# Performance work log

Hardware: AMD Instinct MI355X
Metric: run time of the kernel (lower is better)

The kernel has to match this reference:

```python
import jax, jax.numpy as jnp
import numpy as np

N = 100000       # nodes
E = 1600000      # edges (before self-loops)
IN = 32          # input_dim
HID = 64         # hidden_dim
HEADS = 4
HO = HID // HEADS  # per-head out of gat1
OUT = 32         # output_dim
HID2 = HID // 2
BN_EPS = 1e-5
NEG_SLOPE = 0.2  # PyG GATConv default leaky relu slope


def setup_inputs() -> dict:
    key = jax.random.key(0)
    ks = jax.random.split(key, 28)
    f32 = jnp.float32
    rn = lambda k, s, sc=0.1: jax.random.normal(k, s, f32) * sc
    inp = {}
    inp["x"] = jax.random.normal(ks[0], (N, IN), f32)
    inp["edge_index"] = jax.random.randint(ks[1], (2, E), 0, N, jnp.int32)
    # GATConv 1: in=IN, heads=HEADS, out/head=HO, concat
    inp["W1"] = rn(ks[2], (IN, HEADS * HO))
    inp["att_src1"] = rn(ks[3], (HEADS, HO))
    inp["att_dst1"] = rn(ks[4], (HEADS, HO))
    inp["b1"] = rn(ks[5], (HEADS * HO,))
    # GATConv 2: in=HID, heads=1, out=OUT, no concat (mean)
    inp["W2"] = rn(ks[6], (HID, OUT))
    inp["att_src2"] = rn(ks[7], (1, OUT))
    inp["att_dst2"] = rn(ks[8], (1, OUT))
    inp["b2"] = rn(ks[9], (OUT,))
    # BatchNorms (inference mode: running stats)
    inp["bn1_g"] = jnp.ones((HID,), f32)
    inp["bn1_b"] = jnp.zeros((HID,), f32)
    inp["bn1_m"] = rn(ks[10], (HID,), 0.1)
    inp["bn1_v"] = jax.random.uniform(ks[11], (HID,), f32, 0.5, 1.5)
    inp["bn2_g"] = jnp.ones((OUT,), f32)
    inp["bn2_b"] = jnp.zeros((OUT,), f32)
    inp["bn2_m"] = rn(ks[12], (OUT,), 0.1)
    inp["bn2_v"] = jax.random.uniform(ks[13], (OUT,), f32, 0.5, 1.5)
    # classifier: OUT -> HID2 -> 3
    inp["cls_w1"] = rn(ks[14], (OUT, HID2))
    inp["cls_b1"] = rn(ks[15], (HID2,))
    inp["cls_w2"] = rn(ks[16], (HID2, 3))
    inp["cls_b2"] = rn(ks[17], (3,))
    inp["reg_w1"] = rn(ks[18], (OUT, HID2))
    inp["reg_b1"] = rn(ks[19], (HID2,))
    inp["reg_w2"] = rn(ks[20], (HID2, 1))
    inp["reg_b2"] = rn(ks[21], (1,))
    return inp


def _segment_softmax(e, seg, n):
    # e: [E, H]; softmax over edges sharing the same destination segment
    m = jax.ops.segment_max(e, seg, num_segments=n)
    ex = jnp.exp(e - m[seg])
    s = jax.ops.segment_sum(ex, seg, num_segments=n)
    return ex / (s[seg] + 1e-16)


def _gat(x, src, dst, W, a_src, a_dst, b, heads, ho, concat):
    n = x.shape[0]
    h = (x @ W).reshape(n, heads, ho)                    # [N,H,F]
    e = (h * a_src).sum(-1)[src] + (h * a_dst).sum(-1)[dst]  # [E,H]
    e = jax.nn.leaky_relu(e, NEG_SLOPE)
    alpha = _segment_softmax(e, dst, n)                  # [E,H]
    out = jax.ops.segment_sum(h[src] * alpha[:, :, None], dst, num_segments=n)
    out = out.reshape(n, heads * ho) if concat else out.mean(axis=1)
    return out + b


def _bn(x, g, b, m, v):
    return (x - m) * jax.lax.rsqrt(v + BN_EPS) * g + b


def reference(x, edge_index, W1, att_src1, att_dst1, b1, W2, att_src2, att_dst2, b2,
              bn1_g, bn1_b, bn1_m, bn1_v, bn2_g, bn2_b, bn2_m, bn2_v,
              cls_w1, cls_b1, cls_w2, cls_b2, reg_w1, reg_b1, reg_w2, reg_b2):
    n = x.shape[0]
    # PyG GATConv default add_self_loops=True
    loops = jnp.arange(n, dtype=edge_index.dtype)
    src = jnp.concatenate([edge_index[0], loops])
    dst = jnp.concatenate([edge_index[1], loops])

    h = _gat(x, src, dst, W1, att_src1, att_dst1, b1, HEADS, HO, True)   # [N, HID]
    h = jax.nn.relu(_bn(h, bn1_g, bn1_b, bn1_m, bn1_v))
    emb = _gat(h, src, dst, W2, att_src2, att_dst2, b2, 1, OUT, False)   # [N, OUT]
    emb = jax.nn.relu(_bn(emb, bn2_g, bn2_b, bn2_m, bn2_v))

    roles = jax.nn.relu(emb @ cls_w1 + cls_b1) @ cls_w2 + cls_b2          # [N, 3]
    energy = jax.nn.relu(emb @ reg_w1 + reg_b1) @ reg_w2 + reg_b2         # [N, 1]
    return emb, roles, energy
```

## Files before the change

kernel.cpp:

```cpp
#include <hip/hip_runtime.h>
#include <hip/hip_bf16.h>

#define NN 100000
#define EE 1600000
#define ETOT (EE + NN)
#define IND 32
#define HIDD 64
#define NHEADS 4
#define OUTD 32
#define HID2D 32

#define BSH 8
#define NBUCK 391
#define CAP 5120
#define EPB 2048
#define NBBIN ((ETOT + EPB - 1) / EPB)
#define NBLIN1 (NN / 8)

typedef unsigned int uint;

__device__ __forceinline__ uint pack2(float a, float b) {
  uint lo = (uint)__bfloat16_as_ushort(__float2bfloat16(a));
  uint hi = (uint)__bfloat16_as_ushort(__float2bfloat16(b));
  return (hi << 16) | lo;
}
__device__ __forceinline__ float lo2f(uint w) { return __uint_as_float(w << 16); }
__device__ __forceinline__ float hi2f(uint w) { return __uint_as_float(w & 0xFFFF0000u); }

__global__ __launch_bounds__(256) void k_pre(
    const int* __restrict__ ei, int* __restrict__ bcur, int* __restrict__ bins,
    const float* __restrict__ x, const float* __restrict__ W1,
    const float* __restrict__ atsrc, const float* __restrict__ atdst,
    uint* __restrict__ h1u, float* __restrict__ as1, float* __restrict__ ad1) {
  __shared__ int cnt[NBUCK];
  __shared__ float Ws[IND * HIDD];
  __shared__ float xs[8 * IND];
  __shared__ float atS[HIDD], atD[HIDD];
  int t = threadIdx.x;
  if (blockIdx.x < NBBIN) {
    for (int i = t; i < NBUCK; i += 256) cnt[i] = 0;
    __syncthreads();
    int base = blockIdx.x * EPB;
    int recs[8], bks[8];
#pragma unroll
    for (int k = 0; k < 8; k++) {
      int i = base + k * 256 + t;
      recs[k] = -1; bks[k] = 0;
      if (i < ETOT) {
        int s, d;
        if (i < EE) { s = ei[i]; d = ei[EE + i]; } else { s = i - EE; d = s; }
        recs[k] = (s << BSH) | (d & ((1 << BSH) - 1));
        bks[k] = d >> BSH;
        atomicAdd(&cnt[bks[k]], 1);
      }
    }
    __syncthreads();
    for (int i = t; i < NBUCK; i += 256) cnt[i] = atomicAdd(&bcur[i], cnt[i]);
    __syncthreads();
#pragma unroll
    for (int k = 0; k < 8; k++) {
      if (recs[k] >= 0) {
        int pos = atomicAdd(&cnt[bks[k]], 1);
        bins[bks[k] * CAP + pos] = recs[k];
      }
    }
  } else {
    int bid = blockIdx.x - NBBIN;
    for (int i = t; i < IND * HIDD; i += 256) Ws[i] = W1[i];
    if (t < HIDD) { atS[t] = atsrc[t]; atD[t] = atdst[t]; }
    xs[t] = x[bid * 256 + t];
    __syncthreads();
    int nl = t >> 5, tl = t & 31;
    int node = bid * 8 + nl;
    int j0 = 2 * tl, j1 = j0 + 1;
    float a0 = 0.f, a1 = 0.f;
#pragma unroll
    for (int k = 0; k < IND; k++) {
      float xv = xs[nl * IND + k];
      a0 += xv * Ws[k * HIDD + j0];
      a1 += xv * Ws[k * HIDD + j1];
    }
    h1u[node * 32 + tl] = pack2(a0, a1);
    float ps = a0 * atS[j0] + a1 * atS[j1];
    float pd = a0 * atD[j0] + a1 * atD[j1];
#pragma unroll
    for (int off = 4; off >= 1; off >>= 1) {
      ps += __shfl_down(ps, off, 8);
      pd += __shfl_down(pd, off, 8);
    }
    if ((tl & 7) == 0) {
      as1[node * NHEADS + (tl >> 3)] = ps;
      ad1[node * NHEADS + (tl >> 3)] = pd;
    }
  }
}

__global__ __launch_bounds__(256) void k_lin2(
    const float* __restrict__ hbn, const float* __restrict__ W2,
    const float* __restrict__ atsrc, const float* __restrict__ atdst,
    uint* __restrict__ h2u, float* __restrict__ as2, float* __restrict__ ad2) {
  __shared__ float Ws[HIDD * OUTD];
  __shared__ float xs[16 * HIDD];
  __shared__ float atS[OUTD], atD[OUTD];
  int t = threadIdx.x;
  for (int i = t; i < HIDD * OUTD; i += 256) Ws[i] = W2[i];
  if (t < OUTD) { atS[t] = atsrc[t]; atD[t] = atdst[t]; }
  for (int i = t; i < 16 * HIDD; i += 256) xs[i] = hbn[blockIdx.x * 16 * HIDD + i];
  __syncthreads();
  int nl = t >> 4, tl = t & 15;
  int node = blockIdx.x * 16 + nl;
  int j0 = 2 * tl, j1 = j0 + 1;
  float a0 = 0.f, a1 = 0.f;
#pragma unroll
  for (int k = 0; k < HIDD; k++) {
    float xv = xs[nl * HIDD + k];
    a0 += xv * Ws[k * OUTD + j0];
    a1 += xv * Ws[k * OUTD + j1];
  }
  h2u[node * 16 + tl] = pack2(a0, a1);
  float ps = a0 * atS[j0] + a1 * atS[j1];
  float pd = a0 * atD[j0] + a1 * atD[j1];
#pragma unroll
  for (int off = 8; off >= 1; off >>= 1) {
    ps += __shfl_down(ps, off, 16);
    pd += __shfl_down(pd, off, 16);
  }
  if (tl == 0) { as2[node] = ps; ad2[node] = pd; }
}

__global__ __launch_bounds__(256) void k_csr(const int* __restrict__ bcur,
                                             const int* __restrict__ bins,
                                             int* __restrict__ rowp,
                                             int* __restrict__ srcs) {
  __shared__ int lrec[CAP];
  __shared__ int sA[512], sB[512];
  __shared__ int ldeg[256];
  int b = blockIdx.x, t = threadIdx.x;
  if (b == 0) {
    if (t < 64) srcs[ETOT + t] = 0;
    if (t == 0) rowp[NN] = ETOT;
  }
  sA[t] = (t < NBUCK) ? bcur[t] : 0;
  sA[t + 256] = (t + 256 < NBUCK) ? bcur[t + 256] : 0;
  __syncthreads();
  int* in = sA; int* out = sB;
  for (int off = 1; off < 512; off <<= 1) {
    for (int i = t; i < 512; i += 256)
      out[i] = in[i] + ((i >= off) ? in[i - off] : 0);
    __syncthreads();
    int* tmp = in; in = out; out = tmp;
  }
  int gb = (b == 0) ? 0 : in[b - 1];
  __syncthreads();
  int count = bcur[b]; if (count > CAP) count = CAP;
  ldeg[t] = 0;
  __syncthreads();
  for (int i = t; i < count; i += 256) {
    int r = bins[b * CAP + i];
    lrec[i] = r;
    atomicAdd(&ldeg[r & 255], 1);
  }
  __syncthreads();
  int dv = ldeg[t];
  sA[t] = dv;
  __syncthreads();
  in = sA; out = sB;
  for (int off = 1; off < 256; off <<= 1) {
    out[t] = in[t] + ((t >= off) ? in[t - off] : 0);
    __syncthreads();
    int* tmp = in; in = out; out = tmp;
  }
  int nb = b << BSH;
  int ex = in[t] - dv;
  if (nb + t < NN) rowp[nb + t] = gb + ex;
  ldeg[t] = ex;
  __syncthreads();
  for (int i = t; i < count; i += 256) {
    int r = lrec[i];
    int pos = atomicAdd(&ldeg[r & 255], 1);
    srcs[gb + pos] = (r >> BSH) << 3;
  }
}

__global__ __launch_bounds__(256, 4) void k_agg1(
    const int* __restrict__ rowp, const int* __restrict__ srcs,
    const uint* __restrict__ h1u, const float* __restrict__ as1,
    const float* __restrict__ ad1, const float* __restrict__ b1,
    const float* __restrict__ g, const float* __restrict__ bb,
    const float* __restrict__ m, const float* __restrict__ v,
    float* __restrict__ hbn) {
  int t = threadIdx.x;
  int wid = t >> 6, lane = t & 63;
  int nA = blockIdx.x * 8 + wid * 2;
  int nB = nA + 1;
  int slot = lane >> 3;
  int fl = lane & 7;
  int hd = fl >> 1;
  int stA = rowp[nA], eA = rowp[nA + 1], eB = rowp[nB + 1];
  int stB = eA;
  float advA = ad1[nA * NHEADS + hd];
  float advB = ad1[nB * NHEADS + hd];
  const uint4* h14 = (const uint4*)h1u;
  float accA[8] = {0,0,0,0,0,0,0,0}, accB[8] = {0,0,0,0,0,0,0,0};
  float lA = 0.f, lB = 0.f;
  int pA = stA + slot, pB = stB + slot;
  int sA0 = srcs[pA];
  int sB0 = srcs[pB];
  uint4 wA = h14[sA0 + fl];
  uint4 wB = h14[sB0 + fl];
  float asA = as1[(sA0 >> 1) + hd];
  float asB = as1[(sB0 >> 1) + hd];
  int p1A = pA + 8, p1B = pB + 8;
  int sA1 = srcs[p1A];
  int sB1 = srcs[p1B];
  while (pA < eA || pB < eB) {
    uint4 wnA = h14[sA1 + fl];
    uint4 wnB = h14[sB1 + fl];
    float anA = as1[(sA1 >> 1) + hd];
    float anB = as1[(sB1 >> 1) + hd];
    int p2A = p1A + 8, p2B = p1B + 8;
    int sA2 = srcs[p2A < ETOT ? p2A : ETOT];
    int sB2 = srcs[p2B < ETOT ? p2B : ETOT];
    if (pA < eA) {
      float e = asA + advA;
      e = fmaxf(e, 0.2f * e);
      float ex = __expf(e);
      lA += ex;
      accA[0] += ex * lo2f(wA.x); accA[1] += ex * hi2f(wA.x);
      accA[2] += ex * lo2f(wA.y); accA[3] += ex * hi2f(wA.y);
      accA[4] += ex * lo2f(wA.z); accA[5] += ex * hi2f(wA.z);
      accA[6] += ex * lo2f(wA.w); accA[7] += ex * hi2f(wA.w);
    }
    if (pB < eB) {
      float e = asB + advB;
      e = fmaxf(e, 0.2f * e);
      float ex = __expf(e);
      lB += ex;
      accB[0] += ex * lo2f(wB.x); accB[1] += ex * hi2f(wB.x);
      accB[2] += ex * lo2f(wB.y); accB[3] += ex * hi2f(wB.y);
      accB[4] += ex * lo2f(wB.z); accB[5] += ex * hi2f(wB.z);
      accB[6] += ex * lo2f(wB.w); accB[7] += ex * hi2f(wB.w);
    }
    wA = wnA; wB = wnB; asA = anA; asB = anB;
    sA1 = sA2; sB1 = sB2;
    pA = p1A; pB = p1B; p1A = p2A; p1B = p2B;
  }
#pragma unroll
  for (int off = 8; off <= 32; off <<= 1) {
#pragma unroll
    for (int i = 0; i < 8; i++) {
      accA[i] += __shfl_xor(accA[i], off, 64);
      accB[i] += __shfl_xor(accB[i], off, 64);
    }
    lA += __shfl_xor(lA, off, 64);
    lB += __shfl_xor(lB, off, 64);
  }
  if (slot < 2) {
    int node = slot == 0 ? nA : nB;
    float lsum = slot == 0 ? lA : lB;
    float li = 1.f / (lsum + 1e-16f);
    int fb = fl * 8;
    float o[8];
#pragma unroll
    for (int i = 0; i < 8; i++) {
      int j = fb + i;
      float av = slot == 0 ? accA[i] : accB[i];
      float ov = av * li + b1[j];
      ov = (ov - m[j]) * rsqrtf(v[j] + 1e-5f) * g[j] + bb[j];
      o[i] = fmaxf(ov, 0.f);
    }
    float4* dst = (float4*)(hbn + node * HIDD + fb);
    dst[0] = make_float4(o[0], o[1], o[2], o[3]);
    dst[1] = make_float4(o[4], o[5], o[6], o[7]);
  }
}

__global__ __launch_bounds__(256, 4) void k_agg2(
    const int* __restrict__ rowp, const int* __restrict__ srcs,
    const uint* __restrict__ h2u, const float* __restrict__ as2,
    const float* __restrict__ ad2, const float* __restrict__ b2v,
    const float* __restrict__ g, const float* __restrict__ bb,
    const float* __restrict__ m, const float* __restrict__ v,
    float* __restrict__ out_emb) {
  int t = threadIdx.x;
  int wid = t >> 6, lane = t & 63;
  int nA = blockIdx.x * 8 + wid * 2;
  int nB = nA + 1;
  int slot = lane >> 3;
  int fl = lane & 7;
  int stA = rowp[nA], eA = rowp[nA + 1], eB = rowp[nB + 1];
  int stB = eA;
  float advA = ad2[nA], advB = ad2[nB];
  const uint2* h22 = (const uint2*)h2u;
  float accA[4] = {0,0,0,0}, accB[4] = {0,0,0,0};
  float lA = 0.f, lB = 0.f;
  int pA = stA + slot, pB = stB + slot;
  int sA0 = srcs[pA];
  int sB0 = srcs[pB];
  uint2 wA = h22[sA0 + fl];
  uint2 wB = h22[sB0 + fl];
  float asA = as2[sA0 >> 3], asB = as2[sB0 >> 3];
  int p1A = pA + 8, p1B = pB + 8;
  int sA1 = srcs[p1A];
  int sB1 = srcs[p1B];
  while (pA < eA || pB < eB) {
    uint2 wnA = h22[sA1 + fl];
    uint2 wnB = h22[sB1 + fl];
    float anA = as2[sA1 >> 3], anB = as2[sB1 >> 3];
    int p2A = p1A + 8, p2B = p1B + 8;
    int sA2 = srcs[p2A < ETOT ? p2A : ETOT];
    int sB2 = srcs[p2B < ETOT ? p2B : ETOT];
    if (pA < eA) {
      float e = asA + advA;
      e = fmaxf(e, 0.2f * e);
      float ex = __expf(e);
      lA += ex;
      accA[0] += ex * lo2f(wA.x); accA[1] += ex * hi2f(wA.x);
      accA[2] += ex * lo2f(wA.y); accA[3] += ex * hi2f(wA.y);
    }
    if (pB < eB) {
      float e = asB + advB;
      e = fmaxf(e, 0.2f * e);
      float ex = __expf(e);
      lB += ex;
      accB[0] += ex * lo2f(wB.x); accB[1] += ex * hi2f(wB.x);
      accB[2] += ex * lo2f(wB.y); accB[3] += ex * hi2f(wB.y);
    }
    wA = wnA; wB = wnB; asA = anA; asB = anB;
    sA1 = sA2; sB1 = sB2;
    pA = p1A; pB = p1B; p1A = p2A; p1B = p2B;
  }
#pragma unroll
  for (int off = 8; off <= 32; off <<= 1) {
#pragma unroll
    for (int i = 0; i < 4; i++) {
      accA[i] += __shfl_xor(accA[i], off, 64);
      accB[i] += __shfl_xor(accB[i], off, 64);
    }
    lA += __shfl_xor(lA, off, 64);
    lB += __shfl_xor(lB, off, 64);
  }
  if (slot < 2) {
    int node = slot == 0 ? nA : nB;
    float lsum = slot == 0 ? lA : lB;
    float li = 1.f / (lsum + 1e-16f);
    int fb = fl * 4;
    float o[4];
#pragma unroll
    for (int i = 0; i < 4; i++) {
      int j = fb + i;
      float av = slot == 0 ? accA[i] : accB[i];
      float ov = av * li + b2v[j];
      ov = (ov - m[j]) * rsqrtf(v[j] + 1e-5f) * g[j] + bb[j];
      o[i] = fmaxf(ov, 0.f);
    }
    *(float4*)(out_emb + node * OUTD + fb) = make_float4(o[0], o[1], o[2], o[3]);
  }
}

__global__ __launch_bounds__(256) void k_mlp(
    const float* __restrict__ embf,
    const float* __restrict__ cw1, const float* __restrict__ cb1,
    const float* __restrict__ cw2, const float* __restrict__ cb2,
    const float* __restrict__ rw1, const float* __restrict__ rb1,
    const float* __restrict__ rw2, const float* __restrict__ rb2,
    float* __restrict__ out_roles, float* __restrict__ out_energy) {
  __shared__ float C1[OUTD * HID2D], R1[OUTD * HID2D];
  __shared__ float C2[HID2D * 3], CB1[HID2D], RB1[HID2D], R2[HID2D];
  __shared__ float CB2v[3], RB2v;
  int t = threadIdx.x;
  for (int i = t; i < OUTD * HID2D; i += 256) { C1[i] = cw1[i]; R1[i] = rw1[i]; }
  if (t < HID2D) { CB1[t] = cb1[t]; RB1[t] = rb1[t]; R2[t] = rw2[t]; }
  if (t < HID2D * 3) C2[t] = cw2[t];
  if (t < 3) CB2v[t] = cb2[t];
  if (t == 0) RB2v = rb2[0];
  __syncthreads();
  int node = blockIdx.x * 256 + t;
  if (node >= NN) return;
  float e[OUTD];
#pragma unroll
  for (int k = 0; k < OUTD; k++) e[k] = embf[node * OUTD + k];
  float r0 = CB2v[0], r1 = CB2v[1], r2 = CB2v[2], en = RB2v;
  for (int j = 0; j < HID2D; j++) {
    float hc = CB1[j], hr = RB1[j];
#pragma unroll
    for (int k = 0; k < OUTD; k++) {
      hc += e[k] * C1[k * HID2D + j];
      hr += e[k] * R1[k * HID2D + j];
    }
    hc = fmaxf(hc, 0.f);
    hr = fmaxf(hr, 0.f);
    r0 += hc * C2[j * 3 + 0];
    r1 += hc * C2[j * 3 + 1];
    r2 += hc * C2[j * 3 + 2];
    en += hr * R2[j];
  }
  out_roles[node * 3 + 0] = r0;
  out_roles[node * 3 + 1] = r1;
  out_roles[node * 3 + 2] = r2;
  out_energy[node] = en;
}

extern "C" void kernel_launch(void* const* d_in, const int* in_sizes, int n_in,
                              void* d_out, int out_size, void* d_ws, size_t ws_size,
                              hipStream_t stream) {
  const float* x    = (const float*)d_in[0];
  const int*   ei   = (const int*)d_in[1];
  const float* W1   = (const float*)d_in[2];
  const float* as1w = (const float*)d_in[3];
  const float* ad1w = (const float*)d_in[4];
  const float* b1   = (const float*)d_in[5];
  const float* W2   = (const float*)d_in[6];
  const float* as2w = (const float*)d_in[7];
  const float* ad2w = (const float*)d_in[8];
  const float* b2v  = (const float*)d_in[9];
  const float* bn1g = (const float*)d_in[10];
  const float* bn1b = (const float*)d_in[11];
  const float* bn1m = (const float*)d_in[12];
  const float* bn1v = (const float*)d_in[13];
  const float* bn2g = (const float*)d_in[14];
  const float* bn2b = (const float*)d_in[15];
  const float* bn2m = (const float*)d_in[16];
  const float* bn2v = (const float*)d_in[17];
  const float* cw1  = (const float*)d_in[18];
  const float* cb1  = (const float*)d_in[19];
  const float* cw2  = (const float*)d_in[20];
  const float* cb2  = (const float*)d_in[21];
  const float* rw1  = (const float*)d_in[22];
  const float* rb1  = (const float*)d_in[23];
  const float* rw2  = (const float*)d_in[24];
  const float* rb2  = (const float*)d_in[25];

  uint*  h1u = (uint*)d_ws;
  float* hbn = (float*)(h1u + NN * 32);
  float* as1 = hbn + NN * HIDD;
  float* ad1 = as1 + NN * NHEADS;
  int* rowp  = (int*)(ad1 + NN * NHEADS);
  int* srcs  = rowp + NN + 1;
  int* bcur  = srcs + ETOT + 64;
  int* bins  = bcur + 512;
  uint* h2u  = h1u;
  float* as2 = as1;
  float* ad2 = ad1;

  float* out        = (float*)d_out;
  float* out_emb    = out;
  float* out_roles  = out + NN * OUTD;
  float* out_energy = out + NN * (OUTD + 3);

  hipMemsetAsync(bcur, 0, 512 * sizeof(int), stream);
  k_pre<<<NBBIN + NBLIN1, 256, 0, stream>>>(ei, bcur, bins, x, W1, as1w, ad1w, h1u, as1, ad1);
  k_csr<<<NBUCK, 256, 0, stream>>>(bcur, bins, rowp, srcs);
  k_agg1<<<NN / 8, 256, 0, stream>>>(rowp, srcs, h1u, as1, ad1, b1, bn1g, bn1b, bn1m, bn1v, hbn);
  k_lin2<<<NN / 16, 256, 0, stream>>>(hbn, W2, as2w, ad2w, h2u, as2, ad2);
  k_agg2<<<NN / 8, 256, 0, stream>>>(rowp, srcs, h2u, as2, ad2, b2v, bn2g, bn2b, bn2m, bn2v, out_emb);
  k_mlp<<<(NN + 255) / 256, 256, 0, stream>>>(out_emb, cw1, cb1, cw2, cb2, rw1, rb1, rw2, rb2, out_roles, out_energy);
}
```

Before: 330.5 us.

## Split fused binning/linear kernel into separate bin and lin1 kernels with larger edge chunks

Replaces the combined k_pre kernel, which mixed edge-binning blocks and layer-1 linear blocks in one launch, with a dedicated k_bin kernel and a separate k_lin1 kernel launched after CSR construction. k_bin processes 8192 edges per block in a strided loop, re-reading the edge indices in its second pass instead of holding them in registers, so fewer blocks contend on the global bucket counters. The split adds one kernel launch, gives up the overlap between binning and the linear transform, and doubles edge-index reads.

```diff
diff --git a/kernel.cpp b/kernel.cpp
--- a/kernel.cpp
+++ b/kernel.cpp
@@ -13,9 +13,7 @@
 #define BSH 8
 #define NBUCK 391
 #define CAP 5120
-#define EPB 2048
-#define NBBIN ((ETOT + EPB - 1) / EPB)
-#define NBLIN1 (NN / 8)
+#define EPB 8192
 
 typedef unsigned int uint;
 
@@ -27,71 +25,39 @@
 __device__ __forceinline__ float lo2f(uint w) { return __uint_as_float(w << 16); }
 __device__ __forceinline__ float hi2f(uint w) { return __uint_as_float(w & 0xFFFF0000u); }
 
-__global__ __launch_bounds__(256) void k_pre(
-    const int* __restrict__ ei, int* __restrict__ bcur, int* __restrict__ bins,
+__global__ __launch_bounds__(256) void k_lin1(
     const float* __restrict__ x, const float* __restrict__ W1,
     const float* __restrict__ atsrc, const float* __restrict__ atdst,
     uint* __restrict__ h1u, float* __restrict__ as1, float* __restrict__ ad1) {
-  __shared__ int cnt[NBUCK];
   __shared__ float Ws[IND * HIDD];
   __shared__ float xs[8 * IND];
   __shared__ float atS[HIDD], atD[HIDD];
   int t = threadIdx.x;
-  if (blockIdx.x < NBBIN) {
-    for (int i = t; i < NBUCK; i += 256) cnt[i] = 0;
-    __syncthreads();
-    int base = blockIdx.x * EPB;
-    int recs[8], bks[8];
-#pragma unroll
-    for (int k = 0; k < 8; k++) {
-      int i = base + k * 256 + t;
-      recs[k] = -1; bks[k] = 0;
-      if (i < ETOT) {
-        int s, d;
-        if (i < EE) { s = ei[i]; d = ei[EE + i]; } else { s = i - EE; d = s; }
-        recs[k] = (s << BSH) | (d & ((1 << BSH) - 1));
-        bks[k] = d >> BSH;
-        atomicAdd(&cnt[bks[k]], 1);
-      }
-    }
-    __syncthreads();
-    for (int i = t; i < NBUCK; i += 256) cnt[i] = atomicAdd(&bcur[i], cnt[i]);
-    __syncthreads();
-#pragma unroll
-    for (int k = 0; k < 8; k++) {
-      if (recs[k] >= 0) {
-        int pos = atomicAdd(&cnt[bks[k]], 1);
-        bins[bks[k] * CAP + pos] = recs[k];
-      }
-    }
-  } else {
-    int bid = blockIdx.x - NBBIN;
-    for (int i = t; i < IND * HIDD; i += 256) Ws[i] = W1[i];
-    if (t < HIDD) { atS[t] = atsrc[t]; atD[t] = atdst[t]; }
-    xs[t] = x[bid * 256 + t];
-    __syncthreads();
-    int nl = t >> 5, tl = t & 31;
-    int node = bid * 8 + nl;
-    int j0 = 2 * tl, j1 = j0 + 1;
-    float a0 = 0.f, a1 = 0.f;
-#pragma unroll
-    for (int k = 0; k < IND; k++) {
-      float xv = xs[nl * IND + k];
-      a0 += xv * Ws[k * HIDD + j0];
-      a1 += xv * Ws[k * HIDD + j1];
-    }
-    h1u[node * 32 + tl] = pack2(a0, a1);
-    float ps = a0 * atS[j0] + a1 * atS[j1];
-    float pd = a0 * atD[j0] + a1 * atD[j1];
-#pragma unroll
-    for (int off = 4; off >= 1; off >>= 1) {
-      ps += __shfl_down(ps, off, 8);
-      pd += __shfl_down(pd, off, 8);
-    }
-    if ((tl & 7) == 0) {
-      as1[node * NHEADS + (tl >> 3)] = ps;
-      ad1[node * NHEADS + (tl >> 3)] = pd;
-    }
+  for (int i = t; i < IND * HIDD; i += 256) Ws[i] = W1[i];
+  if (t < HIDD) { atS[t] = atsrc[t]; atD[t] = atdst[t]; }
+  xs[t] = x[blockIdx.x * 256 + t];
+  __syncthreads();
+  int nl = t >> 5, tl = t & 31;
+  int node = blockIdx.x * 8 + nl;
+  int j0 = 2 * tl, j1 = j0 + 1;
+  float a0 = 0.f, a1 = 0.f;
+#pragma unroll
+  for (int k = 0; k < IND; k++) {
+    float xv = xs[nl * IND + k];
+    a0 += xv * Ws[k * HIDD + j0];
+    a1 += xv * Ws[k * HIDD + j1];
+  }
+  h1u[node * 32 + tl] = pack2(a0, a1);
+  float ps = a0 * atS[j0] + a1 * atS[j1];
+  float pd = a0 * atD[j0] + a1 * atD[j1];
+#pragma unroll
+  for (int off = 4; off >= 1; off >>= 1) {
+    ps += __shfl_down(ps, off, 8);
+    pd += __shfl_down(pd, off, 8);
+  }
+  if ((tl & 7) == 0) {
+    as1[node * NHEADS + (tl >> 3)] = ps;
+    ad1[node * NHEADS + (tl >> 3)] = pd;
   }
 }
 
@@ -126,6 +92,31 @@
     pd += __shfl_down(pd, off, 16);
   }
   if (tl == 0) { as2[node] = ps; ad2[node] = pd; }
+}
+
+__global__ __launch_bounds__(256) void k_bin(const int* __restrict__ ei,
+                                             int* __restrict__ bcur,
+                                             int* __restrict__ bins) {
+  __shared__ int cnt[NBUCK];
+  int t = threadIdx.x;
+  for (int i = t; i < NBUCK; i += 256) cnt[i] = 0;
+  __syncthreads();
+  int base = blockIdx.x * EPB;
+  int lim = base + EPB; if (lim > ETOT) lim = ETOT;
+  for (int i = base + t; i < lim; i += 256) {
+    int d = (i < EE) ? ei[EE + i] : (i - EE);
+    atomicAdd(&cnt[d >> BSH], 1);
+  }
+  __syncthreads();
+  for (int i = t; i < NBUCK; i += 256) cnt[i] = atomicAdd(&bcur[i], cnt[i]);
+  __syncthreads();
+  for (int i = base + t; i < lim; i += 256) {
+    int s, d;
+    if (i < EE) { s = ei[i]; d = ei[EE + i]; } else { s = i - EE; d = s; }
+    int bk = d >> BSH;
+    int pos = atomicAdd(&cnt[bk], 1);
+    bins[bk * CAP + pos] = (s << BSH) | (d & ((1 << BSH) - 1));
+  }
 }
 
 __global__ __launch_bounds__(256) void k_csr(const int* __restrict__ bcur,
@@ -449,8 +440,9 @@
   float* out_energy = out + NN * (OUTD + 3);
 
   hipMemsetAsync(bcur, 0, 512 * sizeof(int), stream);
-  k_pre<<<NBBIN + NBLIN1, 256, 0, stream>>>(ei, bcur, bins, x, W1, as1w, ad1w, h1u, as1, ad1);
+  k_bin<<<(ETOT + EPB - 1) / EPB, 256, 0, stream>>>(ei, bcur, bins);
   k_csr<<<NBUCK, 256, 0, stream>>>(bcur, bins, rowp, srcs);
+  k_lin1<<<NN / 8, 256, 0, stream>>>(x, W1, as1w, ad1w, h1u, as1, ad1);
   k_agg1<<<NN / 8, 256, 0, stream>>>(rowp, srcs, h1u, as1, ad1, b1, bn1g, bn1b, bn1m, bn1v, hbn);
   k_lin2<<<NN / 16, 256, 0, stream>>>(hbn, W2, as2w, ad2w, h2u, as2, ad2);
   k_agg2<<<NN / 8, 256, 0, stream>>>(rowp, srcs, h2u, as2, ad2, b2v, bn2g, bn2b, bn2m, bn2v, out_emb);
```

New measurement: 327.3 us. No clear change (-1.0%).
